# Kernel optimization log

Hardware: AMD Instinct MI355X
Metric: run time of the kernel (lower is better)

The kernel has to match this reference:

```python
import jax, jax.numpy as jnp
import numpy as np

EPS = 1e-6  # VNLeakyReLU eps
NORM_EPS = 1e-12  # F.normalize default eps
NEG_SLOPE = 0.2


def _normalize(v):
    # matches torch F.normalize(p=2, dim=-1): v / max(||v||, eps)
    n = jnp.linalg.norm(v, axis=-1, keepdims=True)
    return v / jnp.maximum(n, NORM_EPS)


def _bgs_extended(d6s):
    # d6s: [B,N,D,3,2] -> rotation matrices [B,N,D,3,3] (columns b1,b2,b3)
    b1 = _normalize(d6s[..., 0])
    a2 = d6s[..., 1]
    proj = jnp.sum(b1 * a2, axis=-1, keepdims=True) * b1
    b2 = _normalize(a2 - proj)
    b3 = jnp.cross(b1, b2)
    return jnp.stack([b1, b2, b3], axis=-1)


def setup_inputs() -> dict:
    key = jax.random.key(0)
    kX, kJ, kA, kB, kC, kW = jax.random.split(key, 6)
    B, N, Din, Dout = 8, 4096, 128, 256
    return {
        "X": jax.random.normal(kX, (B, N, Din, 3), dtype=jnp.float32),
        "J": jax.random.normal(kJ, (B, N, Din, 3, 2), dtype=jnp.float32),
        "Amat": jax.random.normal(kA, (Dout, Din), dtype=jnp.float32),
        "Bmat": jax.random.normal(kB, (Dout, Din), dtype=jnp.float32),
        "Cmat": jax.random.normal(kC, (Dout, Din), dtype=jnp.float32),
        "Wdir": jax.random.normal(kW, (Dout, Dout), dtype=jnp.float32),
        "device": 0,
    }


def reference(X, J, Amat, Bmat, Cmat, Wdir, device):
    # ---- Affine_Linear_Abla_wocomplex ----
    R = _bgs_extended(J)  # [B,N,D,3,3]
    # get_rtx(k, RT, X) = sum_j R[...,j,k] * X[...,j]; stacking k=0,1,2 gives:
    a_term = jnp.einsum('bndjk,bndj->bndk', R, X)  # [B,N,D,3]
    # Y = A@a + B@a + C@a == (A+B+C)@a  (einsum 'fe,bcei->bcfi')
    Y = jnp.einsum('fe,bnei->bnfi', Amat + Bmat + Cmat, a_term)  # [B,N,F,3]
    # ---- permute(0,2,3,1) -> [B, F, 3, N] ----
    x = jnp.transpose(Y, (0, 2, 3, 1))
    # ---- VNLeakyReLU ----
    d = jnp.einsum('oc,bcin->boin', Wdir, x)
    dot = jnp.sum(x * d, axis=2, keepdims=True)
    mask = (dot >= 0).astype(x.dtype)
    d_norm_sq = jnp.sum(d * d, axis=2, keepdims=True)
    x_out = NEG_SLOPE * x + (1 - NEG_SLOPE) * (
        mask * x + (1 - mask) * (x - dot / (d_norm_sq + EPS) * d)
    )
    return x_out  # [B, F, 3, N]
```

## Files before the change

kernel.cpp:

```cpp
#include <hip/hip_runtime.h>

#define TT 16
#define NBLK 2048
#define LDA 136
#define LDY 264

typedef short s16x8 __attribute__((ext_vector_type(8)));
typedef float f32x4 __attribute__((ext_vector_type(4)));

__device__ __forceinline__ unsigned short f2bf(float f) {
  union { float f; unsigned u; } v; v.f = f;
  unsigned r = v.u + 0x7FFFu + ((v.u >> 16) & 1u);
  return (unsigned short)(r >> 16);
}
__device__ __forceinline__ float bf2f(unsigned short h) {
  union { unsigned u; float f; } v; v.u = ((unsigned)h) << 16;
  return v.f;
}
__device__ __forceinline__ void split2(float x, unsigned short& h, unsigned short& m) {
  h = f2bf(x);
  m = f2bf(x - bf2f(h));
}

__global__ __launch_bounds__(256) void prep_kernel(
    const float* __restrict__ A, const float* __restrict__ Bm,
    const float* __restrict__ C, const float* __restrict__ W,
    unsigned short* __restrict__ M3h, unsigned short* __restrict__ M3m,
    unsigned short* __restrict__ Wh, unsigned short* __restrict__ Wm) {
  int tid = blockIdx.x * 256 + threadIdx.x;
  if (tid < 128 * 256) {
    unsigned short h, m;
    split2(A[tid] + Bm[tid] + C[tid], h, m);
    M3h[tid] = h; M3m[tid] = m;
  } else {
    int t2 = tid - 128 * 256;
    unsigned short h, m;
    split2(W[t2], h, m);
    Wh[t2] = h; Wm[t2] = m;
  }
}

__global__ __launch_bounds__(512, 4) void affine_vnrelu_mfma(
    const float* __restrict__ X, const float* __restrict__ J,
    const unsigned short* __restrict__ M3h, const unsigned short* __restrict__ M3m,
    const unsigned short* __restrict__ Wh, const unsigned short* __restrict__ Wm,
    float* __restrict__ out) {
  __shared__ unsigned short smem[2 * 48 * LDY];
  unsigned short* aTh = smem;
  unsigned short* aTm = smem + 48 * LDA;

  const int tid = threadIdx.x;
  const int lane = tid & 63;
  const int w = tid >> 6;
  const int quad = lane >> 4;
  const int nl = lane & 15;
  const long g0 = (long)blockIdx.x * TT;
  const int b = (int)(g0 >> 12);
  const int n0 = (int)(g0 & 4095);

  #pragma unroll
  for (int k = 0; k < 4; ++k) {
    int p = k * 512 + tid;
    int t = p >> 7;
    int dch = p & 127;
    long base = (g0 + t) * 128 + dch;
    const float* Xp = X + base * 3;
    const float* Jp = J + base * 6;
    float x0 = Xp[0], x1 = Xp[1], x2 = Xp[2];
    float j0 = Jp[0], j1 = Jp[1], j2 = Jp[2], j3 = Jp[3], j4 = Jp[4], j5 = Jp[5];
    float c00 = j0, c01 = j2, c02 = j4;
    float a20 = j1, a21 = j3, a22 = j5;
    float n1 = sqrtf(c00 * c00 + c01 * c01 + c02 * c02);
    float inv1 = 1.0f / fmaxf(n1, 1e-12f);
    float b10 = c00 * inv1, b11 = c01 * inv1, b12 = c02 * inv1;
    float pr = b10 * a20 + b11 * a21 + b12 * a22;
    float u0 = a20 - pr * b10, u1 = a21 - pr * b11, u2 = a22 - pr * b12;
    float n2 = sqrtf(u0 * u0 + u1 * u1 + u2 * u2);
    float inv2 = 1.0f / fmaxf(n2, 1e-12f);
    float b20 = u0 * inv2, b21 = u1 * inv2, b22 = u2 * inv2;
    float b30 = b11 * b22 - b12 * b21;
    float b31 = b12 * b20 - b10 * b22;
    float b32 = b10 * b21 - b11 * b20;
    unsigned short h, m;
    int r0 = t * LDA + dch;
    split2(b10 * x0 + b11 * x1 + b12 * x2, h, m); aTh[r0] = h; aTm[r0] = m;
    int r1 = (16 + t) * LDA + dch;
    split2(b20 * x0 + b21 * x1 + b22 * x2, h, m); aTh[r1] = h; aTm[r1] = m;
    int r2 = (32 + t) * LDA + dch;
    split2(b30 * x0 + b31 * x1 + b32 * x2, h, m); aTh[r2] = h; aTm[r2] = m;
  }
  __syncthreads();

  const int f0 = w * 32;
  const f32x4 zz = {0.f, 0.f, 0.f, 0.f};

  f32x4 acc1[3][2];
  #pragma unroll
  for (int mt = 0; mt < 3; ++mt)
    #pragma unroll
    for (int nt = 0; nt < 2; ++nt) acc1[mt][nt] = zz;

  #pragma unroll 2
  for (int ks = 0; ks < 4; ++ks) {
    int e0 = ks * 32 + quad * 8;
    s16x8 bh[2], bm[2];
    #pragma unroll
    for (int nt = 0; nt < 2; ++nt) {
      int bo = (f0 + nt * 16 + nl) * 128 + e0;
      bh[nt] = *(const s16x8*)(M3h + bo);
      bm[nt] = *(const s16x8*)(M3m + bo);
    }
    #pragma unroll
    for (int mt = 0; mt < 3; ++mt) {
      int ao = (mt * 16 + nl) * LDA + e0;
      s16x8 ah = *(const s16x8*)(aTh + ao);
      s16x8 am = *(const s16x8*)(aTm + ao);
      #pragma unroll
      for (int nt = 0; nt < 2; ++nt) {
        f32x4 a = acc1[mt][nt];
        a = __builtin_amdgcn_mfma_f32_16x16x32_bf16(ah, bh[nt], a, 0, 0, 0);
        a = __builtin_amdgcn_mfma_f32_16x16x32_bf16(ah, bm[nt], a, 0, 0, 0);
        a = __builtin_amdgcn_mfma_f32_16x16x32_bf16(am, bh[nt], a, 0, 0, 0);
        acc1[mt][nt] = a;
      }
    }
  }
  __syncthreads();

  unsigned short* Yth = smem;
  unsigned short* Ytm = smem + 48 * LDY;
  #pragma unroll
  for (int mt = 0; mt < 3; ++mt)
    #pragma unroll
    for (int nt = 0; nt < 2; ++nt)
      #pragma unroll
      for (int r = 0; r < 4; ++r) {
        unsigned short h, m;
        split2(acc1[mt][nt][r], h, m);
        int yo = (mt * 16 + quad * 4 + r) * LDY + f0 + nt * 16 + nl;
        Yth[yo] = h; Ytm[yo] = m;
      }
  __syncthreads();

  f32x4 acc2[3][2];
  #pragma unroll
  for (int mt = 0; mt < 3; ++mt)
    #pragma unroll
    for (int nt = 0; nt < 2; ++nt) acc2[mt][nt] = zz;

  #pragma unroll 2
  for (int ks = 0; ks < 8; ++ks) {
    int c0 = ks * 32 + quad * 8;
    s16x8 bh[2], bm[2];
    #pragma unroll
    for (int nt = 0; nt < 2; ++nt) {
      int bo = (f0 + nt * 16 + nl) * 256 + c0;
      bh[nt] = *(const s16x8*)(Wh + bo);
      bm[nt] = *(const s16x8*)(Wm + bo);
    }
    #pragma unroll
    for (int mt = 0; mt < 3; ++mt) {
      int ao = (mt * 16 + nl) * LDY + c0;
      s16x8 ah = *(const s16x8*)(Yth + ao);
      s16x8 am = *(const s16x8*)(Ytm + ao);
      #pragma unroll
      for (int nt = 0; nt < 2; ++nt) {
        f32x4 a = acc2[mt][nt];
        a = __builtin_amdgcn_mfma_f32_16x16x32_bf16(ah, bh[nt], a, 0, 0, 0);
        a = __builtin_amdgcn_mfma_f32_16x16x32_bf16(ah, bm[nt], a, 0, 0, 0);
        a = __builtin_amdgcn_mfma_f32_16x16x32_bf16(am, bh[nt], a, 0, 0, 0);
        acc2[mt][nt] = a;
      }
    }
  }

  #pragma unroll
  for (int nt = 0; nt < 2; ++nt) {
    int f = f0 + nt * 16 + nl;
    float* ob = out + ((long)(b * 256 + f) * 3) * 4096 + n0 + quad * 4;
    float o[3][4];
    #pragma unroll
    for (int r = 0; r < 4; ++r) {
      float x0 = acc1[0][nt][r], x1 = acc1[1][nt][r], x2 = acc1[2][nt][r];
      float d0 = acc2[0][nt][r], d1 = acc2[1][nt][r], d2 = acc2[2][nt][r];
      float dot = x0 * d0 + x1 * d1 + x2 * d2;
      float dn = d0 * d0 + d1 * d1 + d2 * d2;
      float s = (dot < 0.0f) ? (0.8f * dot / (dn + 1e-6f)) : 0.0f;
      o[0][r] = x0 - s * d0;
      o[1][r] = x1 - s * d1;
      o[2][r] = x2 - s * d2;
    }
    #pragma unroll
    for (int i = 0; i < 3; ++i)
      *(float4*)(ob + ((long)i * 4096)) = make_float4(o[i][0], o[i][1], o[i][2], o[i][3]);
  }
}

extern "C" void kernel_launch(void* const* d_in, const int* in_sizes, int n_in,
                              void* d_out, int out_size, void* d_ws, size_t ws_size,
                              hipStream_t stream) {
  const float* X = (const float*)d_in[0];
  const float* J = (const float*)d_in[1];
  const float* A = (const float*)d_in[2];
  const float* B = (const float*)d_in[3];
  const float* C = (const float*)d_in[4];
  const float* W = (const float*)d_in[5];
  unsigned short* M3h = (unsigned short*)d_ws;
  unsigned short* M3m = M3h + 128 * 256;
  unsigned short* Wh  = M3m + 128 * 256;
  unsigned short* Wm  = Wh + 256 * 256;
  float* out = (float*)d_out;

  prep_kernel<<<(128 * 256 + 256 * 256) / 256, 256, 0, stream>>>(
      A, B, C, W, M3h, M3m, Wh, Wm);
  affine_vnrelu_mfma<<<NBLK, 512, 0, stream>>>(
      X, J, M3h, M3m, Wh, Wm, out);
}
```

Before: 306.5 us.

## Raise occupancy target, prefetch first weight fragments, reload x from LDS

Raises the launch-bounds occupancy hint from 4 to 6 waves per SIMD, fully unrolls both MFMA k-loops, and issues the first global weight-fragment loads before each barrier so their latency overlaps the sync. To free registers, the first GEMM's accumulators are no longer kept through the second GEMM; x is rebuilt in the epilogue from the hi/lo bf16 split stored in LDS. This reduces register pressure but makes x slightly less precise (hi+lo bf16 instead of the fp32 accumulator) and adds LDS reads in the epilogue.

```diff
diff --git a/kernel.cpp b/kernel.cpp
--- a/kernel.cpp
+++ b/kernel.cpp
@@ -40,7 +40,7 @@
   }
 }
 
-__global__ __launch_bounds__(512, 4) void affine_vnrelu_mfma(
+__global__ __launch_bounds__(512, 6) void affine_vnrelu_mfma(
     const float* __restrict__ X, const float* __restrict__ J,
     const unsigned short* __restrict__ M3h, const unsigned short* __restrict__ M3m,
     const unsigned short* __restrict__ Wh, const unsigned short* __restrict__ Wm,
@@ -57,6 +57,7 @@
   const long g0 = (long)blockIdx.x * TT;
   const int b = (int)(g0 >> 12);
   const int n0 = (int)(g0 & 4095);
+  const int f0 = w * 32;
 
   #pragma unroll
   for (int k = 0; k < 4; ++k) {
@@ -89,9 +90,16 @@
     int r2 = (32 + t) * LDA + dch;
     split2(b30 * x0 + b31 * x1 + b32 * x2, h, m); aTh[r2] = h; aTm[r2] = m;
   }
+
+  s16x8 p1h[2], p1m[2];
+  #pragma unroll
+  for (int nt = 0; nt < 2; ++nt) {
+    int bo = (f0 + nt * 16 + nl) * 128 + quad * 8;
+    p1h[nt] = *(const s16x8*)(M3h + bo);
+    p1m[nt] = *(const s16x8*)(M3m + bo);
+  }
   __syncthreads();
 
-  const int f0 = w * 32;
   const f32x4 zz = {0.f, 0.f, 0.f, 0.f};
 
   f32x4 acc1[3][2];
@@ -100,15 +108,19 @@
     #pragma unroll
     for (int nt = 0; nt < 2; ++nt) acc1[mt][nt] = zz;
 
-  #pragma unroll 2
+  #pragma unroll
   for (int ks = 0; ks < 4; ++ks) {
     int e0 = ks * 32 + quad * 8;
     s16x8 bh[2], bm[2];
-    #pragma unroll
-    for (int nt = 0; nt < 2; ++nt) {
-      int bo = (f0 + nt * 16 + nl) * 128 + e0;
-      bh[nt] = *(const s16x8*)(M3h + bo);
-      bm[nt] = *(const s16x8*)(M3m + bo);
+    if (ks == 0) {
+      bh[0] = p1h[0]; bh[1] = p1h[1]; bm[0] = p1m[0]; bm[1] = p1m[1];
+    } else {
+      #pragma unroll
+      for (int nt = 0; nt < 2; ++nt) {
+        int bo = (f0 + nt * 16 + nl) * 128 + e0;
+        bh[nt] = *(const s16x8*)(M3h + bo);
+        bm[nt] = *(const s16x8*)(M3m + bo);
+      }
     }
     #pragma unroll
     for (int mt = 0; mt < 3; ++mt) {
@@ -125,6 +137,14 @@
       }
     }
   }
+
+  s16x8 p2h[2], p2m[2];
+  #pragma unroll
+  for (int nt = 0; nt < 2; ++nt) {
+    int bo = (f0 + nt * 16 + nl) * 256 + quad * 8;
+    p2h[nt] = *(const s16x8*)(Wh + bo);
+    p2m[nt] = *(const s16x8*)(Wm + bo);
+  }
   __syncthreads();
 
   unsigned short* Yth = smem;
@@ -148,15 +168,19 @@
     #pragma unroll
     for (int nt = 0; nt < 2; ++nt) acc2[mt][nt] = zz;
 
-  #pragma unroll 2
+  #pragma unroll
   for (int ks = 0; ks < 8; ++ks) {
     int c0 = ks * 32 + quad * 8;
     s16x8 bh[2], bm[2];
-    #pragma unroll
-    for (int nt = 0; nt < 2; ++nt) {
-      int bo = (f0 + nt * 16 + nl) * 256 + c0;
-      bh[nt] = *(const s16x8*)(Wh + bo);
-      bm[nt] = *(const s16x8*)(Wm + bo);
+    if (ks == 0) {
+      bh[0] = p2h[0]; bh[1] = p2h[1]; bm[0] = p2m[0]; bm[1] = p2m[1];
+    } else {
+      #pragma unroll
+      for (int nt = 0; nt < 2; ++nt) {
+        int bo = (f0 + nt * 16 + nl) * 256 + c0;
+        bh[nt] = *(const s16x8*)(Wh + bo);
+        bm[nt] = *(const s16x8*)(Wm + bo);
+      }
     }
     #pragma unroll
     for (int mt = 0; mt < 3; ++mt) {
@@ -181,7 +205,10 @@
     float o[3][4];
     #pragma unroll
     for (int r = 0; r < 4; ++r) {
-      float x0 = acc1[0][nt][r], x1 = acc1[1][nt][r], x2 = acc1[2][nt][r];
+      int row = quad * 4 + r;
+      float x0 = bf2f(Yth[row * LDY + f])        + bf2f(Ytm[row * LDY + f]);
+      float x1 = bf2f(Yth[(16 + row) * LDY + f]) + bf2f(Ytm[(16 + row) * LDY + f]);
+      float x2 = bf2f(Yth[(32 + row) * LDY + f]) + bf2f(Ytm[(32 + row) * LDY + f]);
       float d0 = acc2[0][nt][r], d1 = acc2[1][nt][r], d2 = acc2[2][nt][r];
       float dot = x0 * d0 + x1 * d1 + x2 * d2;
       float dn = d0 * d0 + d1 * d1 + d2 * d2;
```

New measurement: 307.5 us. About the same (+0.3%).

## Split Gram-Schmidt projection into separate vectorized kernel with global bf16 staging

Applied to the files above, without the earlier changes.

Moves the per-channel frame construction and projection into its own kernel. That kernel reads X and J with float4 loads and writes bf16 hi/lo splits of the projected vectors to a workspace laid out per token. The GEMM kernel then loads its A operand straight from global memory instead of LDS, which drops one barrier, and both k-loops are fully unrolled. The aim is to replace the strided scalar loads of the fused kernel with coalesced ones. The cost is an extra round trip of about 50 MB through global memory and one more kernel launch.

```diff
diff --git a/kernel.cpp b/kernel.cpp
--- a/kernel.cpp
+++ b/kernel.cpp
@@ -2,7 +2,6 @@
 
 #define TT 16
 #define NBLK 2048
-#define LDA 136
 #define LDY 264
 
 typedef short s16x8 __attribute__((ext_vector_type(8)));
@@ -40,34 +39,26 @@
   }
 }
 
-__global__ __launch_bounds__(512, 4) void affine_vnrelu_mfma(
+__global__ __launch_bounds__(256) void phaseA_kernel(
     const float* __restrict__ X, const float* __restrict__ J,
-    const unsigned short* __restrict__ M3h, const unsigned short* __restrict__ M3m,
-    const unsigned short* __restrict__ Wh, const unsigned short* __restrict__ Wm,
-    float* __restrict__ out) {
-  __shared__ unsigned short smem[2 * 48 * LDY];
-  unsigned short* aTh = smem;
-  unsigned short* aTm = smem + 48 * LDA;
-
-  const int tid = threadIdx.x;
-  const int lane = tid & 63;
-  const int w = tid >> 6;
-  const int quad = lane >> 4;
-  const int nl = lane & 15;
-  const long g0 = (long)blockIdx.x * TT;
-  const int b = (int)(g0 >> 12);
-  const int n0 = (int)(g0 & 4095);
-
-  #pragma unroll
-  for (int k = 0; k < 4; ++k) {
-    int p = k * 512 + tid;
-    int t = p >> 7;
-    int dch = p & 127;
-    long base = (g0 + t) * 128 + dch;
-    const float* Xp = X + base * 3;
-    const float* Jp = J + base * 6;
-    float x0 = Xp[0], x1 = Xp[1], x2 = Xp[2];
-    float j0 = Jp[0], j1 = Jp[1], j2 = Jp[2], j3 = Jp[3], j4 = Jp[4], j5 = Jp[5];
+    unsigned short* __restrict__ aTh, unsigned short* __restrict__ aTm) {
+  int tid = blockIdx.x * 256 + threadIdx.x;
+  int token = tid >> 5;
+  int dch0 = (tid & 31) * 4;
+  const float* Xp = X + ((long)token * 128 + dch0) * 3;
+  const float* Jp = J + ((long)token * 128 + dch0) * 6;
+  float xf[12], jf[24];
+  #pragma unroll
+  for (int q = 0; q < 3; ++q) *(float4*)(xf + 4 * q) = ((const float4*)Xp)[q];
+  #pragma unroll
+  for (int q = 0; q < 6; ++q) *(float4*)(jf + 4 * q) = ((const float4*)Jp)[q];
+
+  unsigned short hs[3][4], ms[3][4];
+  #pragma unroll
+  for (int e = 0; e < 4; ++e) {
+    float x0 = xf[3 * e], x1 = xf[3 * e + 1], x2 = xf[3 * e + 2];
+    float j0 = jf[6 * e],     j1 = jf[6 * e + 1], j2 = jf[6 * e + 2];
+    float j3 = jf[6 * e + 3], j4 = jf[6 * e + 4], j5 = jf[6 * e + 5];
     float c00 = j0, c01 = j2, c02 = j4;
     float a20 = j1, a21 = j3, a22 = j5;
     float n1 = sqrtf(c00 * c00 + c01 * c01 + c02 * c02);
@@ -81,16 +72,36 @@
     float b30 = b11 * b22 - b12 * b21;
     float b31 = b12 * b20 - b10 * b22;
     float b32 = b10 * b21 - b11 * b20;
-    unsigned short h, m;
-    int r0 = t * LDA + dch;
-    split2(b10 * x0 + b11 * x1 + b12 * x2, h, m); aTh[r0] = h; aTm[r0] = m;
-    int r1 = (16 + t) * LDA + dch;
-    split2(b20 * x0 + b21 * x1 + b22 * x2, h, m); aTh[r1] = h; aTm[r1] = m;
-    int r2 = (32 + t) * LDA + dch;
-    split2(b30 * x0 + b31 * x1 + b32 * x2, h, m); aTh[r2] = h; aTm[r2] = m;
-  }
-  __syncthreads();
-
+    split2(b10 * x0 + b11 * x1 + b12 * x2, hs[0][e], ms[0][e]);
+    split2(b20 * x0 + b21 * x1 + b22 * x2, hs[1][e], ms[1][e]);
+    split2(b30 * x0 + b31 * x1 + b32 * x2, hs[2][e], ms[2][e]);
+  }
+  long rb = (long)token * 384 + dch0;
+  #pragma unroll
+  for (int i = 0; i < 3; ++i) {
+    short4 vh, vm;
+    vh.x = hs[i][0]; vh.y = hs[i][1]; vh.z = hs[i][2]; vh.w = hs[i][3];
+    vm.x = ms[i][0]; vm.y = ms[i][1]; vm.z = ms[i][2]; vm.w = ms[i][3];
+    *(short4*)(aTh + rb + i * 128) = vh;
+    *(short4*)(aTm + rb + i * 128) = vm;
+  }
+}
+
+__global__ __launch_bounds__(512, 4) void gemm_vnrelu(
+    const unsigned short* __restrict__ aTh, const unsigned short* __restrict__ aTm,
+    const unsigned short* __restrict__ M3h, const unsigned short* __restrict__ M3m,
+    const unsigned short* __restrict__ Wh, const unsigned short* __restrict__ Wm,
+    float* __restrict__ out) {
+  __shared__ unsigned short smem[2 * 48 * LDY];
+
+  const int tid = threadIdx.x;
+  const int lane = tid & 63;
+  const int w = tid >> 6;
+  const int quad = lane >> 4;
+  const int nl = lane & 15;
+  const long g0 = (long)blockIdx.x * TT;
+  const int b = (int)(g0 >> 12);
+  const int n0 = (int)(g0 & 4095);
   const int f0 = w * 32;
   const f32x4 zz = {0.f, 0.f, 0.f, 0.f};
 
@@ -100,7 +111,10 @@
     #pragma unroll
     for (int nt = 0; nt < 2; ++nt) acc1[mt][nt] = zz;
 
-  #pragma unroll 2
+  const unsigned short* aThb = aTh + (g0 + nl) * 384;
+  const unsigned short* aTmb = aTm + (g0 + nl) * 384;
+
+  #pragma unroll
   for (int ks = 0; ks < 4; ++ks) {
     int e0 = ks * 32 + quad * 8;
     s16x8 bh[2], bm[2];
@@ -112,9 +126,8 @@
     }
     #pragma unroll
     for (int mt = 0; mt < 3; ++mt) {
-      int ao = (mt * 16 + nl) * LDA + e0;
-      s16x8 ah = *(const s16x8*)(aTh + ao);
-      s16x8 am = *(const s16x8*)(aTm + ao);
+      s16x8 ah = *(const s16x8*)(aThb + mt * 128 + e0);
+      s16x8 am = *(const s16x8*)(aTmb + mt * 128 + e0);
       #pragma unroll
       for (int nt = 0; nt < 2; ++nt) {
         f32x4 a = acc1[mt][nt];
@@ -125,7 +138,6 @@
       }
     }
   }
-  __syncthreads();
 
   unsigned short* Yth = smem;
   unsigned short* Ytm = smem + 48 * LDY;
@@ -148,7 +160,7 @@
     #pragma unroll
     for (int nt = 0; nt < 2; ++nt) acc2[mt][nt] = zz;
 
-  #pragma unroll 2
+  #pragma unroll
   for (int ks = 0; ks < 8; ++ks) {
     int c0 = ks * 32 + quad * 8;
     s16x8 bh[2], bm[2];
@@ -209,10 +221,13 @@
   unsigned short* M3m = M3h + 128 * 256;
   unsigned short* Wh  = M3m + 128 * 256;
   unsigned short* Wm  = Wh + 256 * 256;
+  unsigned short* aTh = Wm + 256 * 256;
+  unsigned short* aTm = aTh + (long)32768 * 384;
   float* out = (float*)d_out;
 
+  phaseA_kernel<<<4096, 256, 0, stream>>>(X, J, aTh, aTm);
   prep_kernel<<<(128 * 256 + 256 * 256) / 256, 256, 0, stream>>>(
       A, B, C, W, M3h, M3m, Wh, Wm);
-  affine_vnrelu_mfma<<<NBLK, 512, 0, stream>>>(
-      X, J, M3h, M3m, Wh, Wm, out);
-}
+  gemm_vnrelu<<<NBLK, 512, 0, stream>>>(
+      aTh, aTm, M3h, M3m, Wh, Wm, out);
+}
```

Measured after the change: 355.9 us. +16.1%, slower.
